# Optimization experiments

Measured on AMD Instinct MI355X. Metric: run time of the kernel, lower is better.

## Reference

```python
import jax, jax.numpy as jnp
import numpy as np

B, N, DIN, DE, NH, DK = 4, 256, 128, 64, 8, 16


def setup_inputs() -> dict:
    key = jax.random.key(0)
    ks = jax.random.split(key, 8)
    s = 0.05
    return {
        "h": jax.random.normal(ks[0], (B, N, DIN), jnp.float32),
        "e": jax.random.normal(ks[1], (B, N, N, DE), jnp.float32),
        "mask": jnp.ones((B, N), jnp.float32),
        "WQ": jax.random.normal(ks[2], (DIN, NH * DK), jnp.float32) * s,
        "WK": jax.random.normal(ks[3], (DIN, NH * DK), jnp.float32) * s,
        "WV": jax.random.normal(ks[4], (DIN, NH * DK), jnp.float32) * s,
        "WE": jax.random.normal(ks[5], (DE, NH * DK), jnp.float32) * s,
        "WE2": jax.random.normal(ks[6], (DE, NH * DK), jnp.float32) * s,
    }


def reference(h, e, mask, WQ, WK, WV, WE, WE2):
    b, n, _ = h.shape
    Q = (h @ WQ).reshape(b, n, NH, DK)
    K = (h @ WK).reshape(b, n, NH, DK) * (float(DK) ** -0.5)
    V = (h @ WV).reshape(b, n, NH, DK)
    E = (e @ WE).reshape(b, n, n, NH, DK)
    E2 = (e @ WE2).reshape(b, n, n, NH, DK)
    # edge-augmented scores: (b, i, j, h, k)
    scores = jnp.einsum('bihk,bjhk->bijh', Q, K)[..., None] + E2
    scores = jnp.exp(jnp.clip(scores, -5.0, 5.0))
    attn_mask = mask[:, :, None, None, None] * mask[:, None, :, None, None]
    scores = scores * attn_mask
    softmax_denom = jnp.clip(scores.sum(axis=2), 1e-6, None)  # (b,i,h,k)
    scores = scores * attn_mask  # attn_dropout p=0.0 -> identity
    out = jnp.einsum('bijhk,bjhk->bihk', scores, V)
    out = out + (scores * E).sum(axis=2)
    out = out / softmax_denom
    return out.reshape(b, n, NH * DK)
```

## Files before the change

kernel.cpp:

```cpp
#include <hip/hip_runtime.h>

#define BB   4
#define NN   256
#define DIN  128
#define DE   64
#define NH   8
#define DK   16
#define CC   128

typedef __attribute__((ext_vector_type(8))) short short8;
typedef __attribute__((ext_vector_type(4))) float f32x4;

__device__ __forceinline__ unsigned short f2bfu(float f) {
    union { float f; unsigned int i; } v; v.f = f;
    unsigned int x = v.i;
    x += 0x7FFFu + ((x >> 16) & 1u);
    return (unsigned short)(x >> 16);
}

__global__ __launch_bounds__(256) void prep_kernel(
    const float* __restrict__ h, const float* __restrict__ WQ,
    const float* __restrict__ WK, const float* __restrict__ WV,
    const float* __restrict__ WE, const float* __restrict__ WE2,
    float* __restrict__ Qw, float* __restrict__ Kw, float* __restrict__ Vw,
    unsigned short* __restrict__ wfrag)
{
    __shared__ float hsh[4 * DIN];
    __shared__ float psum[4 * 1536];
    const int t = threadIdx.x;

    if (blockIdx.x >= 256) {
        const int tid  = (blockIdx.x - 256) * 256 + t;
        const int m    = tid >> 10;
        const int g    = (tid >> 7) & 7;
        const int ks   = (tid >> 6) & 1;
        const int lane = tid & 63;
        const int q4 = lane >> 4, l15 = lane & 15;
        const float* W = m ? WE2 : WE;
        union { uint4 u; unsigned short s[8]; } pk;
        #pragma unroll
        for (int ii = 0; ii < 8; ++ii) {
            const int d = ks * 32 + q4 * 8 + ii;
            pk.s[ii] = f2bfu(W[d * CC + g * 16 + l15]);
        }
        ((uint4*)wfrag)[tid] = pk.u;
        return;
    }

    const int r0 = blockIdx.x * 4;
    hsh[t]       = h[(size_t)r0 * DIN + t];
    hsh[256 + t] = h[(size_t)r0 * DIN + 256 + t];
    __syncthreads();

    const int cp  = t & 63;
    const int qtr = t >> 6;
    float aq[4][2], ak[4][2], av[4][2];
    #pragma unroll
    for (int r = 0; r < 4; ++r) {
        aq[r][0]=aq[r][1]=ak[r][0]=ak[r][1]=av[r][0]=av[r][1]=0.f;
    }
    #pragma unroll 4
    for (int dd = 0; dd < 32; ++dd) {
        const int d = qtr * 32 + dd;
        const float2 fq = ((const float2*)WQ)[d * 64 + cp];
        const float2 fk = ((const float2*)WK)[d * 64 + cp];
        const float2 fv = ((const float2*)WV)[d * 64 + cp];
        #pragma unroll
        for (int r = 0; r < 4; ++r) {
            const float hd = hsh[r * DIN + d];
            aq[r][0] = fmaf(hd, fq.x, aq[r][0]); aq[r][1] = fmaf(hd, fq.y, aq[r][1]);
            ak[r][0] = fmaf(hd, fk.x, ak[r][0]); ak[r][1] = fmaf(hd, fk.y, ak[r][1]);
            av[r][0] = fmaf(hd, fv.x, av[r][0]); av[r][1] = fmaf(hd, fv.y, av[r][1]);
        }
    }
    float* pq = psum + qtr * 1536;
    #pragma unroll
    for (int r = 0; r < 4; ++r) {
        pq[r*384       + 2*cp] = aq[r][0]; pq[r*384       + 2*cp+1] = aq[r][1];
        pq[r*384 + 128 + 2*cp] = ak[r][0]; pq[r*384 + 128 + 2*cp+1] = ak[r][1];
        pq[r*384 + 256 + 2*cp] = av[r][0]; pq[r*384 + 256 + 2*cp+1] = av[r][1];
    }
    __syncthreads();
    #pragma unroll
    for (int k = 0; k < 6; ++k) {
        const int o = k * 256 + t;
        float v = psum[o] + psum[1536 + o] + psum[3072 + o] + psum[4608 + o];
        const int r   = o / 384;
        const int mc  = o - r * 384;
        const int mat = mc >> 7;
        const int c   = mc & 127;
        const size_t idx = (size_t)(r0 + r) * CC + c;
        if      (mat == 0) Qw[idx] = v;
        else if (mat == 1) Kw[idx] = v * 0.25f;
        else               Vw[idx] = v;
    }
}

__global__ __launch_bounds__(512, 6) void attn_kernel(
    const float* __restrict__ e, const float* __restrict__ maskp,
    const unsigned short* __restrict__ wfrag,
    const float* __restrict__ Qw, const float* __restrict__ Kw,
    const float* __restrict__ Vw, float* __restrict__ out)
{
    __shared__ __align__(16) unsigned short esh[NN * DE];
    __shared__ float qk_sh[NN * 9];
    __shared__ float msk_sh[NN];
    __shared__ float qrow_sh[CC];

    const int row  = blockIdx.x;
    const int b    = row >> 8, i = row & 255;
    const int t    = threadIdx.x;
    const int wave = t >> 6, lane = t & 63;
    const int q4   = lane >> 4;
    const int l15  = lane & 15;

    {
        const float4* src = (const float4*)(e + (size_t)row * NN * DE);
        uint4* dst = (uint4*)esh;
        #pragma unroll
        for (int r = 0; r < 4; ++r) {
            const int cidx = r * 512 + t;
            const int j = cidx >> 3, ch = cidx & 7;
            const float4 f0 = src[2 * cidx];
            const float4 f1 = src[2 * cidx + 1];
            union { uint4 u; unsigned short s[8]; } pk;
            pk.s[0]=f2bfu(f0.x); pk.s[1]=f2bfu(f0.y); pk.s[2]=f2bfu(f0.z); pk.s[3]=f2bfu(f0.w);
            pk.s[4]=f2bfu(f1.x); pk.s[5]=f2bfu(f1.y); pk.s[6]=f2bfu(f1.z); pk.s[7]=f2bfu(f1.w);
            dst[j * 8 + (ch ^ (j & 7))] = pk.u;
        }
    }
    if (t < CC) qrow_sh[t] = Qw[(size_t)row * CC + t];
    if (t < NN) msk_sh[t] = maskp[b * NN + t];

    short8 bfragE[2], bfragS[2];
    {
        const uint4* wf = (const uint4*)wfrag;
        #pragma unroll
        for (int ks = 0; ks < 2; ++ks) {
            union { uint4 u; short8 s8; } cv;
            cv.u = wf[((0 * 8 + wave) * 2 + ks) * 64 + lane];
            bfragE[ks] = cv.s8;
            cv.u = wf[((1 * 8 + wave) * 2 + ks) * 64 + lane];
            bfragS[ks] = cv.s8;
        }
    }
    __syncthreads();

    {
        const int j  = t & 255;
        const int hb = (t >> 8) * 4;
        const float4* kr = (const float4*)(Kw + (size_t)(b * NN + j) * CC);
        #pragma unroll
        for (int hh = 0; hh < 4; ++hh) {
            const int hgl = hb + hh;
            float s = 0.f;
            #pragma unroll
            for (int p = 0; p < 4; ++p) {
                const float4 kv = kr[hgl * 4 + p];
                const int qb = hgl * 16 + p * 4;
                s += kv.x * qrow_sh[qb]     + kv.y * qrow_sh[qb + 1]
                   + kv.z * qrow_sh[qb + 2] + kv.w * qrow_sh[qb + 3];
            }
            qk_sh[j * 9 + hgl] = s;
        }
    }
    __syncthreads();

    const float mi = msk_sh[i];
    float acc = 0.f, dnm = 0.f;
    const short8* ep = (const short8*)esh;
    const int g = wave;

    #pragma unroll 2
    for (int s = 0; s < 16; ++s) {
        const int ja = s * 16 + l15;
        const short8 a0 = ep[ja * 8 + ((q4    ) ^ (ja & 7))];
        const short8 a1 = ep[ja * 8 + ((q4 + 4) ^ (ja & 7))];

        float vv[4], qk[4], mm[4], mm2[4];
        {
            const float* vrow = Vw + (size_t)(b*NN + s*16 + q4*4) * CC + g*16 + l15;
            #pragma unroll
            for (int r = 0; r < 4; ++r) vv[r] = vrow[r * CC];
        }
        #pragma unroll
        for (int r = 0; r < 4; ++r) {
            const int jr = s * 16 + q4 * 4 + r;
            qk[r] = qk_sh[jr * 9 + g];
            const float m = mi * msk_sh[jr];
            mm[r] = m; mm2[r] = m * m;
        }

        f32x4 s2 = {0.f,0.f,0.f,0.f}, eE = {0.f,0.f,0.f,0.f};
        s2 = __builtin_amdgcn_mfma_f32_16x16x32_bf16(a0, bfragS[0], s2, 0,0,0);
        s2 = __builtin_amdgcn_mfma_f32_16x16x32_bf16(a1, bfragS[1], s2, 0,0,0);
        eE = __builtin_amdgcn_mfma_f32_16x16x32_bf16(a0, bfragE[0], eE, 0,0,0);
        eE = __builtin_amdgcn_mfma_f32_16x16x32_bf16(a1, bfragE[1], eE, 0,0,0);

        #pragma unroll
        for (int r = 0; r < 4; ++r) {
            float sc = qk[r] + s2[r];
            sc = fminf(5.f, fmaxf(-5.f, sc));
            const float p = __expf(sc);
            dnm += p * mm[r];
            acc = fmaf(p * mm2[r], vv[r] + eE[r], acc);
        }
    }

    acc += __shfl_xor(acc, 16); acc += __shfl_xor(acc, 32);
    dnm += __shfl_xor(dnm, 16); dnm += __shfl_xor(dnm, 32);
    if (lane < 16) {
        out[(size_t)row * CC + g * 16 + lane] = acc / fmaxf(dnm, 1e-6f);
    }
}

extern "C" void kernel_launch(void* const* d_in, const int* in_sizes, int n_in,
                              void* d_out, int out_size, void* d_ws, size_t ws_size,
                              hipStream_t stream)
{
    const float* h    = (const float*)d_in[0];
    const float* e    = (const float*)d_in[1];
    const float* mask = (const float*)d_in[2];
    const float* WQ   = (const float*)d_in[3];
    const float* WK   = (const float*)d_in[4];
    const float* WV   = (const float*)d_in[5];
    const float* WE   = (const float*)d_in[6];
    const float* WE2  = (const float*)d_in[7];

    unsigned short* wfrag = (unsigned short*)d_ws;
    float* Qw = (float*)((char*)d_ws + 32768);
    float* Kw = Qw + BB * NN * CC;
    float* Vw = Kw + BB * NN * CC;

    prep_kernel<<<264, 256, 0, stream>>>(h, WQ, WK, WV, WE, WE2,
                                         Qw, Kw, Vw, wfrag);
    attn_kernel<<<BB*NN, 512, 0, stream>>>(e, mask, wfrag, Qw, Kw, Vw,
                                           (float*)d_out);
}
```

Measured before the change: 138.7 us.

## Process two query rows per block with split-j prefetch pipelining of e

Each attention block now handles two query rows and splits the j dimension into two halves. The second half of e is prefetched into registers with nontemporal loads while the first half is being computed. K and V loads, the QK dot products and the hoisted V registers are shared across both rows, which removes redundant K/V traffic and hides e load latency. The cost is more registers (launch bounds lowered to 4 waves per SIMD), half as many blocks, and extra syncthreads.

```diff
diff --git a/kernel.cpp b/kernel.cpp
--- a/kernel.cpp
+++ b/kernel.cpp
@@ -96,42 +96,52 @@
     }
 }
 
-__global__ __launch_bounds__(512, 6) void attn_kernel(
+__global__ __launch_bounds__(512, 4) void attn_kernel(
     const float* __restrict__ e, const float* __restrict__ maskp,
     const unsigned short* __restrict__ wfrag,
     const float* __restrict__ Qw, const float* __restrict__ Kw,
     const float* __restrict__ Vw, float* __restrict__ out)
 {
-    __shared__ __align__(16) unsigned short esh[NN * DE];
-    __shared__ float qk_sh[NN * 9];
-    __shared__ float msk_sh[NN];
-    __shared__ float qrow_sh[CC];
-
-    const int row  = blockIdx.x;
-    const int b    = row >> 8, i = row & 255;
+    __shared__ __align__(16) unsigned short esh[2][128 * DE];
+    __shared__ float qk_sh[2][128 * 9];
+    __shared__ float msk1_sh[2][NN];
+    __shared__ float msk2_sh[2][NN];
+    __shared__ __align__(16) float qrow_sh[2][CC];
+
+    const int blk  = blockIdx.x;
+    const int b    = blk >> 7;
+    const int i0   = (blk & 127) * 2;
     const int t    = threadIdx.x;
     const int wave = t >> 6, lane = t & 63;
     const int q4   = lane >> 4;
     const int l15  = lane & 15;
-
-    {
-        const float4* src = (const float4*)(e + (size_t)row * NN * DE);
-        uint4* dst = (uint4*)esh;
-        #pragma unroll
-        for (int r = 0; r < 4; ++r) {
-            const int cidx = r * 512 + t;
-            const int j = cidx >> 3, ch = cidx & 7;
-            const float4 f0 = src[2 * cidx];
-            const float4 f1 = src[2 * cidx + 1];
-            union { uint4 u; unsigned short s[8]; } pk;
-            pk.s[0]=f2bfu(f0.x); pk.s[1]=f2bfu(f0.y); pk.s[2]=f2bfu(f0.z); pk.s[3]=f2bfu(f0.w);
-            pk.s[4]=f2bfu(f1.x); pk.s[5]=f2bfu(f1.y); pk.s[6]=f2bfu(f1.z); pk.s[7]=f2bfu(f1.w);
-            dst[j * 8 + (ch ^ (j & 7))] = pk.u;
-        }
-    }
-    if (t < CC) qrow_sh[t] = Qw[(size_t)row * CC + t];
-    if (t < NN) msk_sh[t] = maskp[b * NN + t];
-
+    const int g    = wave;
+
+    const int tr = t >> 8;
+    const int tt = t & 255;
+
+    const f32x4* erow = (const f32x4*)(e + (size_t)(b * NN + i0 + tr) * NN * DE);
+    uint4* eshv = (uint4*)esh;
+
+    f32x4 pf[4][2];
+    #pragma unroll
+    for (int it = 0; it < 4; ++it) {
+        const int pp = it * 256 + tt;
+        pf[it][0] = __builtin_nontemporal_load(&erow[2 * pp]);
+        pf[it][1] = __builtin_nontemporal_load(&erow[2 * pp + 1]);
+    }
+
+    if (t < NN) {
+        const float mj  = maskp[b * NN + t];
+        const float mi0 = maskp[b * NN + i0];
+        const float mi1 = maskp[b * NN + i0 + 1];
+        const float a0 = mi0 * mj, a1 = mi1 * mj;
+        msk1_sh[0][t] = a0;  msk2_sh[0][t] = a0 * a0;
+        msk1_sh[1][t] = a1;  msk2_sh[1][t] = a1 * a1;
+    }
+    if (t < 256) {
+        qrow_sh[t >> 7][t & 127] = Qw[(size_t)(b * NN + i0 + (t >> 7)) * CC + (t & 127)];
+    }
     short8 bfragE[2], bfragS[2];
     {
         const uint4* wf = (const uint4*)wfrag;
@@ -144,73 +154,121 @@
             bfragS[ks] = cv.s8;
         }
     }
-    __syncthreads();
-
-    {
-        const int j  = t & 255;
-        const int hb = (t >> 8) * 4;
-        const float4* kr = (const float4*)(Kw + (size_t)(b * NN + j) * CC);
-        #pragma unroll
-        for (int hh = 0; hh < 4; ++hh) {
-            const int hgl = hb + hh;
-            float s = 0.f;
-            #pragma unroll
-            for (int p = 0; p < 4; ++p) {
-                const float4 kv = kr[hgl * 4 + p];
-                const int qb = hgl * 16 + p * 4;
-                s += kv.x * qrow_sh[qb]     + kv.y * qrow_sh[qb + 1]
-                   + kv.z * qrow_sh[qb + 2] + kv.w * qrow_sh[qb + 3];
-            }
-            qk_sh[j * 9 + hgl] = s;
-        }
-    }
-    __syncthreads();
-
-    const float mi = msk_sh[i];
-    float acc = 0.f, dnm = 0.f;
+
+#define EWRITE() {                                                             \
+        _Pragma("unroll")                                                      \
+        for (int it = 0; it < 4; ++it) {                                       \
+            const int pp = it * 256 + tt;                                      \
+            const int jl = pp >> 3, ch8 = pp & 7;                              \
+            union { uint4 u; unsigned short s[8]; } pk;                        \
+            pk.s[0]=f2bfu(pf[it][0][0]); pk.s[1]=f2bfu(pf[it][0][1]);          \
+            pk.s[2]=f2bfu(pf[it][0][2]); pk.s[3]=f2bfu(pf[it][0][3]);          \
+            pk.s[4]=f2bfu(pf[it][1][0]); pk.s[5]=f2bfu(pf[it][1][1]);          \
+            pk.s[6]=f2bfu(pf[it][1][2]); pk.s[7]=f2bfu(pf[it][1][3]);          \
+            eshv[tr * 1024 + jl * 8 + (ch8 ^ (jl & 7))] = pk.u;                \
+        } }
+    EWRITE();
+    __syncthreads();
+
+    #pragma unroll
+    for (int it = 0; it < 4; ++it) {
+        const int pp = it * 256 + tt;
+        pf[it][0] = __builtin_nontemporal_load(&erow[2048 + 2 * pp]);
+        pf[it][1] = __builtin_nontemporal_load(&erow[2048 + 2 * pp + 1]);
+    }
+    __builtin_amdgcn_sched_barrier(0);
+
+    const float* vbase = Vw + ((size_t)(b * NN) + q4 * 4) * CC + g * 16 + l15;
+    float vr[8][4];
+
+#define QK_HALF(H) {                                                           \
+        const int q = t & 31;                                                  \
+        const int hq = q >> 2;                                                 \
+        const float4 qv0 = ((const float4*)qrow_sh[0])[q];                     \
+        const float4 qv1 = ((const float4*)qrow_sh[1])[q];                     \
+        const float4* kb = (const float4*)(Kw + (size_t)(b * NN + (H)*128) * CC); \
+        _Pragma("unroll 4")                                                    \
+        for (int it = 0; it < 8; ++it) {                                       \
+            const int c = it * 512 + t;                                        \
+            const int jl = c >> 5;                                             \
+            const float4 kv = kb[c];                                           \
+            float p0 = kv.x*qv0.x + kv.y*qv0.y + kv.z*qv0.z + kv.w*qv0.w;      \
+            float p1 = kv.x*qv1.x + kv.y*qv1.y + kv.z*qv1.z + kv.w*qv1.w;      \
+            p0 += __shfl_xor(p0, 1); p0 += __shfl_xor(p0, 2);                  \
+            p1 += __shfl_xor(p1, 1); p1 += __shfl_xor(p1, 2);                  \
+            if ((t & 3) == 0) {                                                \
+                qk_sh[0][jl * 9 + hq] = p0;                                    \
+                qk_sh[1][jl * 9 + hq] = p1;                                    \
+            }                                                                  \
+        } }
+
+#define VHOIST(H) {                                                            \
+        _Pragma("unroll")                                                      \
+        for (int s = 0; s < 8; ++s)                                            \
+            _Pragma("unroll")                                                  \
+            for (int r = 0; r < 4; ++r)                                        \
+                vr[s][r] = vbase[((H)*128 + s * 16 + r) * CC];                 \
+        }
+
+    QK_HALF(0); VHOIST(0);
+    __builtin_amdgcn_sched_barrier(0);
+    __syncthreads();
+
+    float acc[2] = {0.f, 0.f}, dnm[2] = {0.f, 0.f};
     const short8* ep = (const short8*)esh;
-    const int g = wave;
-
-    #pragma unroll 2
-    for (int s = 0; s < 16; ++s) {
-        const int ja = s * 16 + l15;
-        const short8 a0 = ep[ja * 8 + ((q4    ) ^ (ja & 7))];
-        const short8 a1 = ep[ja * 8 + ((q4 + 4) ^ (ja & 7))];
-
-        float vv[4], qk[4], mm[4], mm2[4];
-        {
-            const float* vrow = Vw + (size_t)(b*NN + s*16 + q4*4) * CC + g*16 + l15;
-            #pragma unroll
-            for (int r = 0; r < 4; ++r) vv[r] = vrow[r * CC];
-        }
-        #pragma unroll
-        for (int r = 0; r < 4; ++r) {
-            const int jr = s * 16 + q4 * 4 + r;
-            qk[r] = qk_sh[jr * 9 + g];
-            const float m = mi * msk_sh[jr];
-            mm[r] = m; mm2[r] = m * m;
-        }
-
-        f32x4 s2 = {0.f,0.f,0.f,0.f}, eE = {0.f,0.f,0.f,0.f};
-        s2 = __builtin_amdgcn_mfma_f32_16x16x32_bf16(a0, bfragS[0], s2, 0,0,0);
-        s2 = __builtin_amdgcn_mfma_f32_16x16x32_bf16(a1, bfragS[1], s2, 0,0,0);
-        eE = __builtin_amdgcn_mfma_f32_16x16x32_bf16(a0, bfragE[0], eE, 0,0,0);
-        eE = __builtin_amdgcn_mfma_f32_16x16x32_bf16(a1, bfragE[1], eE, 0,0,0);
-
-        #pragma unroll
-        for (int r = 0; r < 4; ++r) {
-            float sc = qk[r] + s2[r];
-            sc = fminf(5.f, fmaxf(-5.f, sc));
-            const float p = __expf(sc);
-            dnm += p * mm[r];
-            acc = fmaf(p * mm2[r], vv[r] + eE[r], acc);
-        }
-    }
-
-    acc += __shfl_xor(acc, 16); acc += __shfl_xor(acc, 32);
-    dnm += __shfl_xor(dnm, 16); dnm += __shfl_xor(dnm, 32);
-    if (lane < 16) {
-        out[(size_t)row * CC + g * 16 + lane] = acc / fmaxf(dnm, 1e-6f);
+
+#define COMPUTE_HALF(H) {                                                      \
+        _Pragma("unroll")                                                      \
+        for (int s = 0; s < 8; ++s) {                                          \
+            const int ja = s * 16 + l15;                                       \
+            _Pragma("unroll")                                                  \
+            for (int ri = 0; ri < 2; ++ri) {                                   \
+                const short8 a0 = ep[ri*1024 + ja*8 + ((q4    ) ^ (ja & 7))];  \
+                const short8 a1 = ep[ri*1024 + ja*8 + ((q4 + 4) ^ (ja & 7))];  \
+                f32x4 s2 = {0.f,0.f,0.f,0.f}, eE = {0.f,0.f,0.f,0.f};          \
+                s2 = __builtin_amdgcn_mfma_f32_16x16x32_bf16(a0, bfragS[0], s2, 0,0,0); \
+                s2 = __builtin_amdgcn_mfma_f32_16x16x32_bf16(a1, bfragS[1], s2, 0,0,0); \
+                eE = __builtin_amdgcn_mfma_f32_16x16x32_bf16(a0, bfragE[0], eE, 0,0,0); \
+                eE = __builtin_amdgcn_mfma_f32_16x16x32_bf16(a1, bfragE[1], eE, 0,0,0); \
+                _Pragma("unroll")                                              \
+                for (int rq = 0; rq < 4; ++rq) {                               \
+                    const int jl = s * 16 + q4 * 4 + rq;                       \
+                    const int jg = (H) * 128 + jl;                             \
+                    float sc = qk_sh[ri][jl * 9 + g] + s2[rq];                 \
+                    sc = fminf(5.f, fmaxf(-5.f, sc));                          \
+                    const float p = __expf(sc);                                \
+                    dnm[ri] = fmaf(p, msk1_sh[ri][jg], dnm[ri]);               \
+                    acc[ri] = fmaf(p * msk2_sh[ri][jg], vr[s][rq] + eE[rq], acc[ri]); \
+                }                                                              \
+            }                                                                  \
+        } }
+
+    COMPUTE_HALF(0);
+    __syncthreads();
+
+    EWRITE();
+    __syncthreads();
+
+    QK_HALF(1); VHOIST(1);
+    __builtin_amdgcn_sched_barrier(0);
+    __syncthreads();
+
+    COMPUTE_HALF(1);
+
+#undef COMPUTE_HALF
+#undef VHOIST
+#undef QK_HALF
+#undef EWRITE
+
+    #pragma unroll
+    for (int ri = 0; ri < 2; ++ri) {
+        float a = acc[ri], d = dnm[ri];
+        a += __shfl_xor(a, 16); a += __shfl_xor(a, 32);
+        d += __shfl_xor(d, 16); d += __shfl_xor(d, 32);
+        if (lane < 16) {
+            out[(size_t)(b * NN + i0 + ri) * CC + g * 16 + lane] =
+                a / fmaxf(d, 1e-6f);
+        }
     }
 }
 
@@ -234,6 +292,6 @@
 
     prep_kernel<<<264, 256, 0, stream>>>(h, WQ, WK, WV, WE, WE2,
                                          Qw, Kw, Vw, wfrag);
-    attn_kernel<<<BB*NN, 512, 0, stream>>>(e, mask, wfrag, Qw, Kw, Vw,
-                                           (float*)d_out);
-}
+    attn_kernel<<<BB*NN/2, 512, 0, stream>>>(e, mask, wfrag, Qw, Kw, Vw,
+                                             (float*)d_out);
+}
```

New measurement: 166.6 us. 1.2x slower.
